# Kernel optimization log

Hardware: AMD Instinct MI355X
Metric: run time of the kernel (lower is better)

The kernel has to match this reference:

```python
import jax, jax.numpy as jnp
import numpy as np

NUM_HEADS = 8


def _nearest_idx(x, x_grid):
    # x: [b,n,dx]; x_grid: [b,H,W,dx] regular grid -> flat nearest cell index [b,n]
    b = x.shape[0]
    H, W = x_grid.shape[1], x_grid.shape[2]
    gf = x_grid.reshape(b, H * W, -1)
    lo = gf[:, :1]   # min corner [b,1,dx]
    hi = gf[:, -1:]  # max corner [b,1,dx]
    dims = jnp.asarray([H, W], dtype=x.dtype)
    t = (x - lo) / (hi - lo) * (dims - 1.0)
    idx = jnp.clip(jnp.round(t), 0.0, dims - 1.0).astype(jnp.int32)  # [b,n,2]
    return idx[..., 0] * W + idx[..., 1]


def _cumcount(idx):
    # per-batch cumulative count of each value, in order of appearance
    b, n = idx.shape
    order = jnp.argsort(idx, axis=1, stable=True)
    s = jnp.take_along_axis(idx, order, axis=1)
    ar = jnp.arange(n)
    new_run = jnp.concatenate([jnp.ones((b, 1), bool), s[:, 1:] != s[:, :-1]], axis=1)
    run_start = jax.lax.cummax(jnp.where(new_run, ar, 0), axis=1)
    cc_sorted = (ar - run_start).astype(jnp.int32)
    return jnp.zeros((b, n), jnp.int32).at[jnp.arange(b)[:, None], order].set(cc_sorted)


def _mhca(q_in, kv, mask, Wq, Wk, Wv, Wo):
    # q_in: [B,1,e]; kv: [B,K,e]; mask: [B,K] (True = attend)
    B, K, e = kv.shape
    dh = e // NUM_HEADS
    q = (q_in @ Wq).reshape(B, 1, NUM_HEADS, dh)
    k = (kv @ Wk).reshape(B, K, NUM_HEADS, dh)
    v = (kv @ Wv).reshape(B, K, NUM_HEADS, dh)
    scores = jnp.einsum('bqhd,bkhd->bhqk', q, k) / jnp.sqrt(jnp.asarray(dh, q.dtype))
    scores = jnp.where(mask[:, None, None, :], scores, jnp.finfo(scores.dtype).min)
    attn = jax.nn.softmax(scores, axis=-1)
    out = jnp.einsum('bhqk,bkhd->bqhd', attn, v).reshape(B, 1, e)
    return out @ Wo


def setup_inputs() -> dict:
    key = jax.random.key(0)
    ks = jax.random.split(key, 8)
    b, n, e, H, W = 8, 8192, 128, 64, 64
    x = jax.random.uniform(ks[0], (b, n, 2), jnp.float32)
    z = jax.random.normal(ks[1], (b, n, e), jnp.float32)
    g0 = jnp.linspace(0.0, 1.0, H)
    g1 = jnp.linspace(0.0, 1.0, W)
    mg = jnp.stack(jnp.meshgrid(g0, g1, indexing='ij'), axis=-1)  # [H,W,2]
    x_grid = jnp.broadcast_to(mg, (b, H, W, 2)).astype(jnp.float32)
    z_grid = jax.random.normal(ks[2], (b, H, W, e), jnp.float32)
    latent = jax.random.normal(ks[3], (e,), jnp.float32)
    scale = 1.0 / np.sqrt(e).astype(np.float32)
    Wq = jax.random.normal(ks[4], (e, e), jnp.float32) * scale
    Wk = jax.random.normal(ks[5], (e, e), jnp.float32) * scale
    Wv = jax.random.normal(ks[6], (e, e), jnp.float32) * scale
    Wo = jax.random.normal(ks[7], (e, e), jnp.float32) * scale
    return {"x": x, "z": z, "x_grid": x_grid, "z_grid": z_grid, "latent": latent,
            "Wq": Wq, "Wk": Wk, "Wv": Wv, "Wo": Wo, "max_patch": 20}


def reference(x, z, x_grid, z_grid, latent, Wq, Wk, Wv, Wo, max_patch):
    b, n, e = z.shape
    H, W = x_grid.shape[1], x_grid.shape[2]
    S = H * W
    nearest = _nearest_idx(x, x_grid)                    # [b,n]
    cc = _cumcount(nearest)                              # [b,n]
    bidx = jnp.broadcast_to(jnp.arange(b)[:, None], (b, n))
    valid = cc < max_patch
    slot = jnp.where(valid, cc, 0)
    # ragged scatter: pack each point's z into its grid cell's padded sequence
    joint = jnp.zeros((b, S, max_patch, e), z.dtype)
    joint = joint.at[bidx, nearest, slot].add(z * valid[..., None].astype(z.dtype))
    zg_flat = z_grid.reshape(b, S, e)
    joint = jnp.concatenate([joint, zg_flat[:, :, None, :]], axis=2)  # [b,S,P+1,e]
    counts = jnp.zeros((b, S), jnp.int32).at[bidx, nearest].add(1)
    mask = jnp.arange(max_patch + 1)[None, None, :] < jnp.minimum(counts, max_patch)[..., None]
    mask = mask.at[..., -1].set(True)  # grid token always attended
    joint = joint.reshape(b * S, max_patch + 1, e)
    mask = mask.reshape(b * S, max_patch + 1)
    q = jnp.broadcast_to(latent, (b * S, 1, e))          # z0_grid queries
    zg = _mhca(q, joint, mask, Wq, Wk, Wv, Wo)           # [b*S,1,e]
    zg = zg.reshape(b, H, W, e)
    return x_grid, zg
```

## Files before the change

kernel.cpp:

```cpp
#include <hip/hip_runtime.h>
#include <hip/hip_bf16.h>
#include <cstdint>
#include <cstddef>

#define S_CELLS 4096
#define NB      8
#define NPTS    8192
#define E       128
#define MAXP    20
#define NHEADS  8
#define NPT_ROWS (NB * NPTS)
#define NGR_ROWS (NB * S_CELLS)
#define NTOK     (NPT_ROWS + NGR_ROWS)


typedef __attribute__((ext_vector_type(8))) short bf16x8;
typedef __attribute__((ext_vector_type(4))) float f32x4;
typedef __attribute__((ext_vector_type(4))) unsigned short us4;

__device__ __forceinline__ unsigned short f2bf_bits(float f) {
    unsigned u = __float_as_uint(f);
    unsigned rounded = u + 0x7FFFu + ((u >> 16) & 1u);
    return (unsigned short)(rounded >> 16);
}
__device__ __forceinline__ float bf2f(unsigned short u) {
    return __uint_as_float(((unsigned)u) << 16);
}

__device__ __forceinline__ void stage_w_t(const float* __restrict__ W,
                                          unsigned short (*__restrict__ W_t)[136],
                                          int t) {
    #pragma unroll
    for (int it = 0; it < 16; ++it) {
        int id = t + it * 256;
        int n  = id & 127;
        int kc = id >> 7;
        float w0 = W[(size_t)(4 * kc + 0) * E + n];
        float w1 = W[(size_t)(4 * kc + 1) * E + n];
        float w2 = W[(size_t)(4 * kc + 2) * E + n];
        float w3 = W[(size_t)(4 * kc + 3) * E + n];
        us4 v;
        v.x = f2bf_bits(w0); v.y = f2bf_bits(w1);
        v.z = f2bf_bits(w2); v.w = f2bf_bits(w3);
        *(us4*)&W_t[n][4 * kc] = v;
    }
}

__global__ void __launch_bounds__(256)
k_points(const float* __restrict__ x,
         const float* __restrict__ x_grid,
         const float* __restrict__ latent,
         const float* __restrict__ Wq,
         const float* __restrict__ Wk,
         int* __restrict__ counts,
         int* __restrict__ slots,
         float* __restrict__ A,
         float* __restrict__ out_xgrid) {
    int i = blockIdx.x * 256 + threadIdx.x;
    out_xgrid[i] = x_grid[i];

    int b = i >> 13;
    float x0 = x[(size_t)i * 2 + 0];
    float x1 = x[(size_t)i * 2 + 1];
    int i0 = (int)rintf(x0 * 63.0f);
    int i1 = (int)rintf(x1 * 63.0f);
    i0 = min(max(i0, 0), 63);
    i1 = min(max(i1, 0), 63);
    int cell = b * S_CELLS + i0 * 64 + i1;
    int slot = atomicAdd(&counts[cell], 1);
    if (slot < MAXP) slots[cell * MAXP + slot] = i & (NPTS - 1);

    if (blockIdx.x == 0) {
        __shared__ float lat[E];
        __shared__ float qv[E];
        const int t = threadIdx.x;
        const int j = t & 127;
        if (t < E) lat[t] = latent[t];
        __syncthreads();
        float acc = 0.0f;
        for (int k2 = 0; k2 < E; ++k2) acc += lat[k2] * Wq[k2 * E + j];
        qv[j] = acc;
        __syncthreads();
        const int hb = (t >> 7) * 4;
        for (int h = hb; h < hb + 4; ++h) {
            float a = 0.0f;
            #pragma unroll
            for (int d = 0; d < 16; ++d) a += Wk[j * E + h * 16 + d] * qv[h * 16 + d];
            A[j * NHEADS + h] = a * 0.25f;
        }
    }
}

__device__ __forceinline__ bf16x8 load_afrag_f32(const float* __restrict__ X,
                                                 int row, int kq, int q) {
    const float4* xr = (const float4*)(X + (size_t)row * E);
    float4 lo = xr[kq * 8 + q * 2];
    float4 hi = xr[kq * 8 + q * 2 + 1];
    bf16x8 f;
    f[0] = (short)f2bf_bits(lo.x);
    f[1] = (short)f2bf_bits(lo.y);
    f[2] = (short)f2bf_bits(lo.z);
    f[3] = (short)f2bf_bits(lo.w);
    f[4] = (short)f2bf_bits(hi.x);
    f[5] = (short)f2bf_bits(hi.y);
    f[6] = (short)f2bf_bits(hi.z);
    f[7] = (short)f2bf_bits(hi.w);
    return f;
}

__global__ void __launch_bounds__(256)
k_gemm1(const float* __restrict__ Xz,
        const float* __restrict__ Xg,
        const float* __restrict__ Wv,
        const float* __restrict__ Aw,
        unsigned short* __restrict__ V,
        float* __restrict__ SC) {
    __shared__ unsigned short W_t[144][136];

    const int t = threadIdx.x;
    stage_w_t(Wv, W_t, t);
    for (int idx = t; idx < E * NHEADS; idx += 256) {
        int k = idx >> 3, hh = idx & 7;
        W_t[128 + hh][k] = f2bf_bits(Aw[idx]);
    }
    for (int idx = t; idx < 8 * 136; idx += 256) {
        int rr = idx / 136, cc = idx - rr * 136;
        W_t[136 + rr][cc] = 0;
    }
    __syncthreads();

    const int lane = t & 63;
    const int wv   = t >> 6;
    const int cn   = lane & 15;
    const int q    = lane >> 4;

    const int grow0 = blockIdx.x * 128;
    const float* Xsrc;
    int srow;
    if (blockIdx.x < 512) { Xsrc = Xz; srow = grow0; }
    else                  { Xsrc = Xg; srow = grow0 - 65536; }

    f32x4 acc[2][9];
    #pragma unroll
    for (int mt = 0; mt < 2; ++mt)
        #pragma unroll
        for (int nt = 0; nt < 9; ++nt)
            acc[mt][nt] = f32x4{0.0f, 0.0f, 0.0f, 0.0f};

    #pragma unroll
    for (int kq = 0; kq < 4; ++kq) {
        bf16x8 a[2];
        #pragma unroll
        for (int mt = 0; mt < 2; ++mt)
            a[mt] = load_afrag_f32(Xsrc, srow + wv * 32 + mt * 16 + cn, kq, q);
        #pragma unroll
        for (int nt = 0; nt < 9; ++nt) {
            const bf16x8 b = *(const bf16x8*)&W_t[nt * 16 + cn][kq * 32 + q * 8];
            #pragma unroll
            for (int mt = 0; mt < 2; ++mt)
                acc[mt][nt] = __builtin_amdgcn_mfma_f32_16x16x32_bf16(
                    a[mt], b, acc[mt][nt], 0, 0, 0);
        }
    }

    #pragma unroll
    for (int mt = 0; mt < 2; ++mt) {
        const int rb = grow0 + wv * 32 + mt * 16 + q * 4;
        #pragma unroll
        for (int nt = 0; nt < 8; ++nt)
            #pragma unroll
            for (int r = 0; r < 4; ++r)
                V[(size_t)(rb + r) * E + nt * 16 + cn] = f2bf_bits(acc[mt][nt][r]);
        if (cn < 8) {
            #pragma unroll
            for (int r = 0; r < 4; ++r)
                SC[(size_t)(rb + r) * NHEADS + cn] = acc[mt][8][r];
        }
    }
}

__global__ void __launch_bounds__(256)
k_attn_proj(const int* __restrict__ counts,
            const int* __restrict__ slots,
            const float* __restrict__ SC,
            const unsigned short* __restrict__ V,
            const float* __restrict__ Wo,
            float* __restrict__ zg) {
    __shared__ unsigned short W_t[128][136];
    __shared__ unsigned short X_s[64][136];

    const int t = threadIdx.x;
    stage_w_t(Wo, W_t, t);

    const int lane = t & 63;
    const int wv   = t >> 6;
    const int cell_base = blockIdx.x * 64 + wv * 16;
    const int b    = blockIdx.x >> 6;
    const int base = b * NPTS;
    const int h    = lane >> 3;

    int cnt_all = (lane < 16) ? counts[cell_base + lane] : 0;
    int slw     = (lane < MAXP) ? slots[(size_t)cell_base * MAXP + lane] : 0;

    for (int ci = 0; ci < 16; ++ci) {
        const int cell = cell_base + ci;
        const int m = min(__shfl(cnt_all, ci, 64), MAXP);
        int slw_n = 0;
        if (ci < 15)
            slw_n = (lane < MAXP) ? slots[(size_t)(cell + 1) * MAXP + lane] : 0;

        size_t r0 = (size_t)(NPT_ROWS + cell);
        float mm = SC[r0 * NHEADS + h];
        float ss = 1.0f;
        unsigned v0 = *(const unsigned*)(V + r0 * E + 2 * lane);
        float o0 = bf2f((unsigned short)v0);
        float o1 = bf2f((unsigned short)(v0 >> 16));

        for (int t0 = 0; t0 < m; t0 += 4) {
            float av[4], p0[4], p1[4];
            #pragma unroll
            for (int j = 0; j < 4; ++j) {
                int pt = __shfl(slw, t0 + j, 64);
                bool val = (t0 + j) < m;
                pt = val ? pt : 0;
                size_t r = (size_t)(base + pt);
                float sa = SC[r * NHEADS + h];
                av[j] = val ? sa : -1e30f;
                unsigned vv = *(const unsigned*)(V + r * E + 2 * lane);
                p0[j] = bf2f((unsigned short)vv);
                p1[j] = bf2f((unsigned short)(vv >> 16));
            }
            #pragma unroll
            for (int j = 0; j < 4; ++j) {
                float nm = fmaxf(mm, av[j]);
                float e  = __expf(av[j] - nm);
                float al = __expf(mm - nm);
                ss = ss * al + e;
                o0 = o0 * al + e * p0[j];
                o1 = o1 * al + e * p1[j];
                mm = nm;
            }
        }
        float inv = 1.0f / ss;
        unsigned packed = (unsigned)f2bf_bits(o0 * inv)
                        | ((unsigned)f2bf_bits(o1 * inv) << 16);
        *(unsigned*)&X_s[wv * 16 + ci][2 * lane] = packed;
        slw = slw_n;
    }
    __syncthreads();

    const int cn = lane & 15;
    const int q  = lane >> 4;
    f32x4 acc[8];
    #pragma unroll
    for (int nt = 0; nt < 8; ++nt) acc[nt] = f32x4{0.0f, 0.0f, 0.0f, 0.0f};

    #pragma unroll
    for (int kq = 0; kq < 4; ++kq) {
        bf16x8 a = *(const bf16x8*)&X_s[wv * 16 + cn][kq * 32 + q * 8];
        #pragma unroll
        for (int nt = 0; nt < 8; ++nt) {
            const bf16x8 bb = *(const bf16x8*)&W_t[nt * 16 + cn][kq * 32 + q * 8];
            acc[nt] = __builtin_amdgcn_mfma_f32_16x16x32_bf16(a, bb, acc[nt], 0, 0, 0);
        }
    }

    const int rb = blockIdx.x * 64 + wv * 16 + q * 4;
    #pragma unroll
    for (int nt = 0; nt < 8; ++nt)
        #pragma unroll
        for (int r = 0; r < 4; ++r)
            zg[(size_t)(rb + r) * E + nt * 16 + cn] = acc[nt][r];
}

extern "C" void kernel_launch(void* const* d_in, const int* in_sizes, int n_in,
                              void* d_out, int out_size, void* d_ws, size_t ws_size,
                              hipStream_t stream) {
    const float* x      = (const float*)d_in[0];
    const float* z      = (const float*)d_in[1];
    const float* x_grid = (const float*)d_in[2];
    const float* z_grid = (const float*)d_in[3];
    const float* latent = (const float*)d_in[4];
    const float* Wq     = (const float*)d_in[5];
    const float* Wk     = (const float*)d_in[6];
    const float* Wv     = (const float*)d_in[7];
    const float* Wo     = (const float*)d_in[8];

    char* ws = (char*)d_ws;
    int*            counts = (int*)(ws + 0);
    int*            slots  = (int*)(ws + 131072);
    float*          A      = (float*)(ws + 2752512);
    float*          SC     = (float*)(ws + 2756608);
    unsigned short* V      = (unsigned short*)(ws + 5902336);

    float* out_xgrid = (float*)d_out;
    float* zg        = (float*)d_out + NB * NPTS;

    (void)hipMemsetAsync(counts, 0, NB * S_CELLS * sizeof(int), stream);

    k_points<<<256, 256, 0, stream>>>(x, x_grid, latent, Wq, Wk,
                                      counts, slots, A, out_xgrid);

    k_gemm1<<<768, 256, 0, stream>>>(z, z_grid, Wv, A, V, SC);

    k_attn_proj<<<512, 256, 0, stream>>>(counts, slots, SC, V, Wo, zg);
}
```

Before: 148.4 us.

## Pre-transpose weights to bf16 once in prep kernel and shrink attention blocks

The fp32-to-bf16 transpose of Wv, Wo and the folded Wk·q scores matrix now happens once, in extra blocks of a prep kernel. It writes padded bf16 tiles to workspace, and the GEMM and attention kernels copy them into LDS with straight float4 loads instead of every block re-transposing strided fp32 weights. The attention/projection kernel now handles 16 cells per block instead of 64, which gives 2048 blocks for better parallelism and smaller LDS. Each wave interleaves 4 cells' softmax state and computes two output column tiles. The cost is extra workspace traffic, plus more blocks that each reload the Wo tile.

```diff
diff --git a/kernel.cpp b/kernel.cpp
--- a/kernel.cpp
+++ b/kernel.cpp
@@ -1,5 +1,4 @@
 #include <hip/hip_runtime.h>
-#include <hip/hip_bf16.h>
 #include <cstdint>
 #include <cstddef>
 
@@ -9,14 +8,18 @@
 #define E       128
 #define MAXP    20
 #define NHEADS  8
-#define NPT_ROWS (NB * NPTS)
-#define NGR_ROWS (NB * S_CELLS)
-#define NTOK     (NPT_ROWS + NGR_ROWS)
-
+#define NPT_ROWS 65536
+#define NGR_ROWS 32768
+
+#define WS_COUNTS 0
+#define WS_SLOTS  131072
+#define WS_WT1    2752512
+#define WS_WT2    2793472
+#define WS_SC     2828288
+#define WS_V      5974016
 
 typedef __attribute__((ext_vector_type(8))) short bf16x8;
 typedef __attribute__((ext_vector_type(4))) float f32x4;
-typedef __attribute__((ext_vector_type(4))) unsigned short us4;
 
 __device__ __forceinline__ unsigned short f2bf_bits(float f) {
     unsigned u = __float_as_uint(f);
@@ -27,53 +30,41 @@
     return __uint_as_float(((unsigned)u) << 16);
 }
 
-__device__ __forceinline__ void stage_w_t(const float* __restrict__ W,
-                                          unsigned short (*__restrict__ W_t)[136],
-                                          int t) {
-    #pragma unroll
-    for (int it = 0; it < 16; ++it) {
-        int id = t + it * 256;
-        int n  = id & 127;
-        int kc = id >> 7;
-        float w0 = W[(size_t)(4 * kc + 0) * E + n];
-        float w1 = W[(size_t)(4 * kc + 1) * E + n];
-        float w2 = W[(size_t)(4 * kc + 2) * E + n];
-        float w3 = W[(size_t)(4 * kc + 3) * E + n];
-        us4 v;
-        v.x = f2bf_bits(w0); v.y = f2bf_bits(w1);
-        v.z = f2bf_bits(w2); v.w = f2bf_bits(w3);
-        *(us4*)&W_t[n][4 * kc] = v;
-    }
-}
-
 __global__ void __launch_bounds__(256)
-k_points(const float* __restrict__ x,
-         const float* __restrict__ x_grid,
-         const float* __restrict__ latent,
-         const float* __restrict__ Wq,
-         const float* __restrict__ Wk,
-         int* __restrict__ counts,
-         int* __restrict__ slots,
-         float* __restrict__ A,
-         float* __restrict__ out_xgrid) {
-    int i = blockIdx.x * 256 + threadIdx.x;
-    out_xgrid[i] = x_grid[i];
-
-    int b = i >> 13;
-    float x0 = x[(size_t)i * 2 + 0];
-    float x1 = x[(size_t)i * 2 + 1];
-    int i0 = (int)rintf(x0 * 63.0f);
-    int i1 = (int)rintf(x1 * 63.0f);
-    i0 = min(max(i0, 0), 63);
-    i1 = min(max(i1, 0), 63);
-    int cell = b * S_CELLS + i0 * 64 + i1;
-    int slot = atomicAdd(&counts[cell], 1);
-    if (slot < MAXP) slots[cell * MAXP + slot] = i & (NPTS - 1);
-
-    if (blockIdx.x == 0) {
+k_prep(const float* __restrict__ x,
+       const float* __restrict__ x_grid,
+       const float* __restrict__ latent,
+       const float* __restrict__ Wq,
+       const float* __restrict__ Wk,
+       const float* __restrict__ Wv,
+       const float* __restrict__ Wo,
+       int* __restrict__ counts,
+       int* __restrict__ slots,
+       unsigned short* __restrict__ WT1,
+       unsigned short* __restrict__ WT2,
+       float* __restrict__ out_xgrid) {
+    const int t   = threadIdx.x;
+    const int blk = blockIdx.x;
+
+    if (blk < 256) {
+        int i = blk * 256 + t;
+        out_xgrid[i] = x_grid[i];
+        int b = i >> 13;
+        float x0 = x[(size_t)i * 2 + 0];
+        float x1 = x[(size_t)i * 2 + 1];
+        int i0 = (int)rintf(x0 * 63.0f);
+        int i1 = (int)rintf(x1 * 63.0f);
+        i0 = min(max(i0, 0), 63);
+        i1 = min(max(i1, 0), 63);
+        int cell = b * S_CELLS + i0 * 64 + i1;
+        int slot = atomicAdd(&counts[cell], 1);
+        if (slot < MAXP) slots[(size_t)cell * MAXP + slot] = i & (NPTS - 1);
+        return;
+    }
+
+    if (blk == 256) {
         __shared__ float lat[E];
         __shared__ float qv[E];
-        const int t = threadIdx.x;
         const int j = t & 127;
         if (t < E) lat[t] = latent[t];
         __syncthreads();
@@ -86,7 +77,31 @@
             float a = 0.0f;
             #pragma unroll
             for (int d = 0; d < 16; ++d) a += Wk[j * E + h * 16 + d] * qv[h * 16 + d];
-            A[j * NHEADS + h] = a * 0.25f;
+            WT1[(size_t)(128 + h) * 136 + j] = f2bf_bits(a * 0.25f);
+        }
+        for (int idx = t; idx < 8 * 136; idx += 256) {
+            int rr = idx / 136, cc = idx - rr * 136;
+            WT1[(size_t)(136 + rr) * 136 + cc] = 0;
+        }
+        return;
+    }
+
+    {
+        const float* W = (blk < 261) ? Wv : Wo;
+        unsigned short* WT = (blk < 261) ? WT1 : WT2;
+        const int n0 = ((blk - 257) & 3) * 32;
+        __shared__ float lbuf[128][33];
+        #pragma unroll
+        for (int it = 0; it < 16; ++it) {
+            int k  = (t >> 5) + it * 8;
+            int nl = t & 31;
+            lbuf[k][nl] = W[(size_t)k * E + n0 + nl];
+        }
+        __syncthreads();
+        for (int idx = t; idx < 32 * 136; idx += 256) {
+            int nl = idx / 136, k = idx - nl * 136;
+            float v = (k < 128) ? lbuf[k][nl] : 0.0f;
+            WT[(size_t)(n0 + nl) * 136 + k] = f2bf_bits(v);
         }
     }
 }
@@ -111,21 +126,17 @@
 __global__ void __launch_bounds__(256)
 k_gemm1(const float* __restrict__ Xz,
         const float* __restrict__ Xg,
-        const float* __restrict__ Wv,
-        const float* __restrict__ Aw,
+        const unsigned short* __restrict__ WT1g,
         unsigned short* __restrict__ V,
         float* __restrict__ SC) {
-    __shared__ unsigned short W_t[144][136];
+    __shared__ unsigned short W_t[20480];
 
     const int t = threadIdx.x;
-    stage_w_t(Wv, W_t, t);
-    for (int idx = t; idx < E * NHEADS; idx += 256) {
-        int k = idx >> 3, hh = idx & 7;
-        W_t[128 + hh][k] = f2bf_bits(Aw[idx]);
-    }
-    for (int idx = t; idx < 8 * 136; idx += 256) {
-        int rr = idx / 136, cc = idx - rr * 136;
-        W_t[136 + rr][cc] = 0;
+    {
+        const float4* src = (const float4*)WT1g;
+        float4* dst = (float4*)W_t;
+        #pragma unroll
+        for (int it = 0; it < 10; ++it) dst[t + it * 256] = src[t + it * 256];
     }
     __syncthreads();
 
@@ -138,7 +149,7 @@
     const float* Xsrc;
     int srow;
     if (blockIdx.x < 512) { Xsrc = Xz; srow = grow0; }
-    else                  { Xsrc = Xg; srow = grow0 - 65536; }
+    else                  { Xsrc = Xg; srow = grow0 - NPT_ROWS; }
 
     f32x4 acc[2][9];
     #pragma unroll
@@ -155,7 +166,7 @@
             a[mt] = load_afrag_f32(Xsrc, srow + wv * 32 + mt * 16 + cn, kq, q);
         #pragma unroll
         for (int nt = 0; nt < 9; ++nt) {
-            const bf16x8 b = *(const bf16x8*)&W_t[nt * 16 + cn][kq * 32 + q * 8];
+            const bf16x8 b = *(const bf16x8*)&W_t[(size_t)(nt * 16 + cn) * 136 + kq * 32 + q * 8];
             #pragma unroll
             for (int mt = 0; mt < 2; ++mt)
                 acc[mt][nt] = __builtin_amdgcn_mfma_f32_16x16x32_bf16(
@@ -183,94 +194,107 @@
 k_attn_proj(const int* __restrict__ counts,
             const int* __restrict__ slots,
             const float* __restrict__ SC,
-            const unsigned short* __restrict__ V,
-            const float* __restrict__ Wo,
+            const unsigned short* __restrict__ Vg,
+            const unsigned short* __restrict__ WT2g,
             float* __restrict__ zg) {
-    __shared__ unsigned short W_t[128][136];
-    __shared__ unsigned short X_s[64][136];
+    __shared__ unsigned short W_t[17408];
+    __shared__ unsigned short X_s[16][136];
 
     const int t = threadIdx.x;
-    stage_w_t(Wo, W_t, t);
+    {
+        const float4* src = (const float4*)WT2g;
+        float4* dst = (float4*)W_t;
+        #pragma unroll
+        for (int it = 0; it < 8; ++it) dst[t + it * 256] = src[t + it * 256];
+        if (t < 128) dst[t + 2048] = src[t + 2048];
+    }
 
     const int lane = t & 63;
     const int wv   = t >> 6;
-    const int cell_base = blockIdx.x * 64 + wv * 16;
-    const int b    = blockIdx.x >> 6;
+    const int cb   = blockIdx.x * 16;
+    const int cw   = cb + wv * 4;
+    const int b    = blockIdx.x >> 8;
     const int base = b * NPTS;
     const int h    = lane >> 3;
 
-    int cnt_all = (lane < 16) ? counts[cell_base + lane] : 0;
-    int slw     = (lane < MAXP) ? slots[(size_t)cell_base * MAXP + lane] : 0;
-
-    for (int ci = 0; ci < 16; ++ci) {
-        const int cell = cell_base + ci;
-        const int m = min(__shfl(cnt_all, ci, 64), MAXP);
-        int slw_n = 0;
-        if (ci < 15)
-            slw_n = (lane < MAXP) ? slots[(size_t)(cell + 1) * MAXP + lane] : 0;
-
-        size_t r0 = (size_t)(NPT_ROWS + cell);
-        float mm = SC[r0 * NHEADS + h];
-        float ss = 1.0f;
-        unsigned v0 = *(const unsigned*)(V + r0 * E + 2 * lane);
-        float o0 = bf2f((unsigned short)v0);
-        float o1 = bf2f((unsigned short)(v0 >> 16));
-
+    int cnt_l = (lane < 16) ? counts[cb + lane] : 0;
+
+    int m4[4], sl[4];
+    #pragma unroll
+    for (int ci = 0; ci < 4; ++ci) {
+        m4[ci] = min(__shfl(cnt_l, wv * 4 + ci, 64), MAXP);
+        sl[ci] = (lane < MAXP) ? slots[(size_t)(cw + ci) * MAXP + lane] : 0;
+    }
+
+    float mm[4], ss[4], o0[4], o1[4];
+    #pragma unroll
+    for (int ci = 0; ci < 4; ++ci) {
+        size_t r0 = (size_t)(NPT_ROWS + cw + ci);
+        mm[ci] = SC[r0 * NHEADS + h];
+        unsigned v0 = *(const unsigned*)(Vg + r0 * E + 2 * lane);
+        o0[ci] = bf2f((unsigned short)v0);
+        o1[ci] = bf2f((unsigned short)(v0 >> 16));
+        ss[ci] = 1.0f;
+    }
+
+    #pragma unroll
+    for (int ci = 0; ci < 4; ++ci) {
+        const int m = m4[ci];
         for (int t0 = 0; t0 < m; t0 += 4) {
             float av[4], p0[4], p1[4];
             #pragma unroll
             for (int j = 0; j < 4; ++j) {
-                int pt = __shfl(slw, t0 + j, 64);
+                int pt = __shfl(sl[ci], t0 + j, 64);
                 bool val = (t0 + j) < m;
                 pt = val ? pt : 0;
                 size_t r = (size_t)(base + pt);
                 float sa = SC[r * NHEADS + h];
                 av[j] = val ? sa : -1e30f;
-                unsigned vv = *(const unsigned*)(V + r * E + 2 * lane);
+                unsigned vv = *(const unsigned*)(Vg + r * E + 2 * lane);
                 p0[j] = bf2f((unsigned short)vv);
                 p1[j] = bf2f((unsigned short)(vv >> 16));
             }
             #pragma unroll
             for (int j = 0; j < 4; ++j) {
-                float nm = fmaxf(mm, av[j]);
+                float nm = fmaxf(mm[ci], av[j]);
                 float e  = __expf(av[j] - nm);
-                float al = __expf(mm - nm);
-                ss = ss * al + e;
-                o0 = o0 * al + e * p0[j];
-                o1 = o1 * al + e * p1[j];
-                mm = nm;
+                float al = __expf(mm[ci] - nm);
+                ss[ci] = ss[ci] * al + e;
+                o0[ci] = o0[ci] * al + e * p0[j];
+                o1[ci] = o1[ci] * al + e * p1[j];
+                mm[ci] = nm;
             }
         }
-        float inv = 1.0f / ss;
-        unsigned packed = (unsigned)f2bf_bits(o0 * inv)
-                        | ((unsigned)f2bf_bits(o1 * inv) << 16);
-        *(unsigned*)&X_s[wv * 16 + ci][2 * lane] = packed;
-        slw = slw_n;
+        float inv = 1.0f / ss[ci];
+        unsigned packed = (unsigned)f2bf_bits(o0[ci] * inv)
+                        | ((unsigned)f2bf_bits(o1[ci] * inv) << 16);
+        *(unsigned*)&X_s[wv * 4 + ci][2 * lane] = packed;
     }
     __syncthreads();
 
-    const int cn = lane & 15;
-    const int q  = lane >> 4;
-    f32x4 acc[8];
-    #pragma unroll
-    for (int nt = 0; nt < 8; ++nt) acc[nt] = f32x4{0.0f, 0.0f, 0.0f, 0.0f};
+    const int cn  = lane & 15;
+    const int q   = lane >> 4;
+    const int nt0 = wv * 2;
+    f32x4 acc[2];
+    acc[0] = f32x4{0.0f, 0.0f, 0.0f, 0.0f};
+    acc[1] = f32x4{0.0f, 0.0f, 0.0f, 0.0f};
 
     #pragma unroll
     for (int kq = 0; kq < 4; ++kq) {
-        bf16x8 a = *(const bf16x8*)&X_s[wv * 16 + cn][kq * 32 + q * 8];
-        #pragma unroll
-        for (int nt = 0; nt < 8; ++nt) {
-            const bf16x8 bb = *(const bf16x8*)&W_t[nt * 16 + cn][kq * 32 + q * 8];
-            acc[nt] = __builtin_amdgcn_mfma_f32_16x16x32_bf16(a, bb, acc[nt], 0, 0, 0);
-        }
-    }
-
-    const int rb = blockIdx.x * 64 + wv * 16 + q * 4;
-    #pragma unroll
-    for (int nt = 0; nt < 8; ++nt)
+        bf16x8 a = *(const bf16x8*)&X_s[cn][kq * 32 + q * 8];
+        #pragma unroll
+        for (int j = 0; j < 2; ++j) {
+            const bf16x8 bb = *(const bf16x8*)&W_t[(size_t)((nt0 + j) * 16 + cn) * 136 + kq * 32 + q * 8];
+            acc[j] = __builtin_amdgcn_mfma_f32_16x16x32_bf16(a, bb, acc[j], 0, 0, 0);
+        }
+    }
+
+    const int rb = blockIdx.x * 16 + q * 4;
+    #pragma unroll
+    for (int j = 0; j < 2; ++j)
         #pragma unroll
         for (int r = 0; r < 4; ++r)
-            zg[(size_t)(rb + r) * E + nt * 16 + cn] = acc[nt][r];
+            zg[(size_t)(rb + r) * E + (nt0 + j) * 16 + cn] = acc[j][r];
 }
 
 extern "C" void kernel_launch(void* const* d_in, const int* in_sizes, int n_in,
@@ -287,21 +311,22 @@
     const float* Wo     = (const float*)d_in[8];
 
     char* ws = (char*)d_ws;
-    int*            counts = (int*)(ws + 0);
-    int*            slots  = (int*)(ws + 131072);
-    float*          A      = (float*)(ws + 2752512);
-    float*          SC     = (float*)(ws + 2756608);
-    unsigned short* V      = (unsigned short*)(ws + 5902336);
+    int*            counts = (int*)(ws + WS_COUNTS);
+    int*            slots  = (int*)(ws + WS_SLOTS);
+    unsigned short* WT1    = (unsigned short*)(ws + WS_WT1);
+    unsigned short* WT2    = (unsigned short*)(ws + WS_WT2);
+    float*          SC     = (float*)(ws + WS_SC);
+    unsigned short* V      = (unsigned short*)(ws + WS_V);
 
     float* out_xgrid = (float*)d_out;
     float* zg        = (float*)d_out + NB * NPTS;
 
     (void)hipMemsetAsync(counts, 0, NB * S_CELLS * sizeof(int), stream);
 
-    k_points<<<256, 256, 0, stream>>>(x, x_grid, latent, Wq, Wk,
-                                      counts, slots, A, out_xgrid);
-
-    k_gemm1<<<768, 256, 0, stream>>>(z, z_grid, Wv, A, V, SC);
-
-    k_attn_proj<<<512, 256, 0, stream>>>(counts, slots, SC, V, Wo, zg);
-}
+    k_prep<<<265, 256, 0, stream>>>(x, x_grid, latent, Wq, Wk, Wv, Wo,
+                                    counts, slots, WT1, WT2, out_xgrid);
+
+    k_gemm1<<<768, 256, 0, stream>>>(z, z_grid, WT1, V, SC);
+
+    k_attn_proj<<<2048, 256, 0, stream>>>(counts, slots, SC, V, WT2, zg);
+}
```

After: 139.9 us. 1.06x faster.
